# Kernel tuning notes

Measured on AMD Instinct MI355X. Metric: run time of the kernel, lower is better.

## Reference

```python
import jax, jax.numpy as jnp
import numpy as np

B, N, D, E = 8, 512, 256, 16384  # batch, num_nodes, hidden_dim, num_edges


def setup_inputs() -> dict:
    key = jax.random.key(0)
    kf, ke, k1, k2, k3, k4 = jax.random.split(key, 6)
    features = jax.random.normal(kf, (B, N, D), dtype=jnp.float32)
    edge_index = jax.random.randint(ke, (2, E), 0, N, dtype=jnp.int64)
    # weight_net: Linear(2D -> D), ReLU, Linear(D -> 1), Sigmoid
    s1 = 1.0 / np.sqrt(2 * D)
    s2 = 1.0 / np.sqrt(D)
    W1 = jax.random.uniform(k1, (2 * D, D), jnp.float32, -s1, s1)
    b1 = jax.random.uniform(k2, (D,), jnp.float32, -s1, s1)
    W2 = jax.random.uniform(k3, (D, 1), jnp.float32, -s2, s2)
    b2 = jax.random.uniform(k4, (1,), jnp.float32, -s2, s2)
    return {"features": features, "W1": W1, "b1": b1, "W2": W2, "b2": b2,
            "edge_index": edge_index}


def reference(features, W1, b1, W2, b2, edge_index):
    src, dst = edge_index[0], edge_index[1]            # [E], [E]
    fi = features[:, src]                              # [B, E, D]
    fj = features[:, dst]                              # [B, E, D]
    pair = jnp.concatenate([fi, fj], axis=-1)          # [B, E, 2D]
    h = jax.nn.relu(jnp.einsum('bef,fh->beh', pair, W1) + b1)   # [B, E, D]
    s = jax.nn.sigmoid(jnp.einsum('beh,ho->beo', h, W2) + b2)[..., 0]  # [B, E]
    bsz, n = features.shape[0], features.shape[1]
    weights = jnp.zeros((bsz, n, n), features.dtype).at[:, src, dst].set(s)
    return weights
```

## Files before the change

### kernel.cpp

```cpp
#include <hip/hip_runtime.h>
#include <hip/hip_bf16.h>
#include <cstdint>

#define B_ 8
#define N_ 512
#define D_ 256
#define E_ 16384
#define H_ 256

#define SA_STRIDE 56
#define SB_STRIDE 56
#define BCAP 128

using bf16x8 = __attribute__((ext_vector_type(8))) short;
using f32x4  = __attribute__((ext_vector_type(4))) float;

__device__ inline unsigned short f2bf(float f) {
    union { float f; unsigned u; } v; v.f = f;
    unsigned u = v.u;
    return (unsigned short)((u + 0x7fffu + ((u >> 16) & 1u)) >> 16);
}

__global__ __launch_bounds__(256)
void prep_k(const float* __restrict__ W1, unsigned short* __restrict__ W1T,
            int* __restrict__ gCount) {
    __shared__ float tile[64][65];
    const int tb = blockIdx.x, t = threadIdx.x;
    if (tb == 32) {
        gCount[t] = 0;
        gCount[t + 256] = 0;
        return;
    }
    const int h   = tb >> 4;
    const int rem = tb & 15;
    const int tk  = (rem >> 2) * 64;
    const int tn  = (rem & 3) * 64;
    const float* Wh = W1 + (size_t)h * 256 * 256;
    const int c = t & 63, r0 = t >> 6;
#pragma unroll
    for (int i = 0; i < 16; i++) {
        int r = r0 + i * 4;
        tile[r][c] = Wh[(size_t)(tk + r) * 256 + tn + c];
    }
    __syncthreads();
#pragma unroll
    for (int i = 0; i < 16; i++) {
        int rn = r0 + i * 4;
        W1T[(size_t)(h * 256 + tn + rn) * 256 + tk + c] = f2bf(tile[c][rn]);
    }
}

__global__ __launch_bounds__(256)
void node_gemm(const float* __restrict__ feat,
               const unsigned short* __restrict__ W1T,
               const float* __restrict__ b1,
               const int* __restrict__ eidx,
               unsigned short* __restrict__ P,
               float4* __restrict__ out4,
               int* __restrict__ gCount, int* __restrict__ gBucket) {
    const int t = threadIdx.x;

    if (blockIdx.x >= 128) {
        __shared__ int hist[512];
        __shared__ int base[512];
        const int sb = blockIdx.x - 128;
        int mysrc[8], mydst[8], myslot[8];
        for (int i = t; i < 512; i += 256) hist[i] = 0;
        __syncthreads();
#pragma unroll
        for (int i = 0; i < 8; i++) {
            int e = sb * 2048 + i * 256 + t;
            mysrc[i] = eidx[e];
            mydst[i] = eidx[E_ + e];
            myslot[i] = atomicAdd(&hist[mysrc[i]], 1);
        }
        __syncthreads();
        for (int i = t; i < 512; i += 256) {
            int c = hist[i];
            base[i] = c ? atomicAdd(&gCount[i], c) : 0;
        }
        __syncthreads();
#pragma unroll
        for (int i = 0; i < 8; i++)
            gBucket[(mysrc[i] << 7) + base[mysrc[i]] + myslot[i]] = mydst[i];
        return;
    }

    __shared__ unsigned short sA[64 * SA_STRIDE];
    __shared__ unsigned short sB[256 * SB_STRIDE];

    const int bm = blockIdx.x >> 1;
    const int bn = blockIdx.x & 1;
    const int m0 = bm * 64;

    {
        float4 z = make_float4(0.f, 0.f, 0.f, 0.f);
        float4* oz = out4 + (size_t)blockIdx.x * 4096 + t;
#pragma unroll
        for (int i = 0; i < 16; i++) oz[i * 256] = z;
    }

    const int arow = t >> 2;
    const int akg  = (t & 3) * 8;
    const float* pA = feat + (size_t)(m0 + arow) * 256;
    const unsigned short* pB = W1T + (size_t)(bn * 256 + t) * 256;

    const int wave = t >> 6, lane = t & 63, l15 = lane & 15, quad = lane >> 4;

    f32x4 acc[4][4];
#pragma unroll
    for (int rm = 0; rm < 4; rm++)
#pragma unroll
        for (int cn = 0; cn < 4; cn++)
            acc[rm][cn] = (f32x4){0.f, 0.f, 0.f, 0.f};

    for (int k0 = 0; k0 < 256; k0 += 32) {
        __syncthreads();
        {
            float4 lo = *(const float4*)(pA + k0 + akg);
            float4 hi = *(const float4*)(pA + k0 + akg + 4);
            union { bf16x8 v; unsigned short s[8]; } u;
            u.s[0] = f2bf(lo.x); u.s[1] = f2bf(lo.y); u.s[2] = f2bf(lo.z); u.s[3] = f2bf(lo.w);
            u.s[4] = f2bf(hi.x); u.s[5] = f2bf(hi.y); u.s[6] = f2bf(hi.z); u.s[7] = f2bf(hi.w);
            *(bf16x8*)(sA + arow * SA_STRIDE + akg) = u.v;
        }
        {
            const unsigned short* p = pB + k0;
            uint4 q0 = *(const uint4*)(p);
            uint4 q1 = *(const uint4*)(p + 8);
            uint4 q2 = *(const uint4*)(p + 16);
            uint4 q3 = *(const uint4*)(p + 24);
            *(uint4*)(sB + t * SB_STRIDE +  0) = q0;
            *(uint4*)(sB + t * SB_STRIDE +  8) = q1;
            *(uint4*)(sB + t * SB_STRIDE + 16) = q2;
            *(uint4*)(sB + t * SB_STRIDE + 24) = q3;
        }
        __syncthreads();

        bf16x8 af[4], bfr[4];
#pragma unroll
        for (int rm = 0; rm < 4; rm++)
            af[rm] = *(const bf16x8*)(sA + (rm * 16 + l15) * SA_STRIDE + quad * 8);
#pragma unroll
        for (int cn = 0; cn < 4; cn++)
            bfr[cn] = *(const bf16x8*)(sB + (wave * 64 + cn * 16 + l15) * SB_STRIDE + quad * 8);
#pragma unroll
        for (int rm = 0; rm < 4; rm++)
#pragma unroll
            for (int cn = 0; cn < 4; cn++)
                acc[rm][cn] = __builtin_amdgcn_mfma_f32_16x16x32_bf16(af[rm], bfr[cn], acc[rm][cn], 0, 0, 0);
    }

#pragma unroll
    for (int cn = 0; cn < 4; cn++) {
        int colh = wave * 64 + cn * 16 + l15;
        float bias = (bn == 0) ? b1[colh] : 0.f;
        int col = bn * 256 + colh;
#pragma unroll
        for (int rm = 0; rm < 4; rm++)
#pragma unroll
            for (int r = 0; r < 4; r++) {
                int row = m0 + rm * 16 + quad * 4 + r;
                P[(size_t)row * 512 + col] = f2bf(acc[rm][cn][r] + bias);
            }
    }
}

__device__ inline float dot8nb(uint4 qu, uint4 qv, const float* w2p) {
    unsigned us[4] = {qu.x, qu.y, qu.z, qu.w};
    unsigned vs[4] = {qv.x, qv.y, qv.z, qv.w};
    float p = 0.f;
#pragma unroll
    for (int j = 0; j < 4; j++) {
        float ulo = __uint_as_float(us[j] << 16);
        float uhi = __uint_as_float(us[j] & 0xffff0000u);
        float vlo = __uint_as_float(vs[j] << 16);
        float vhi = __uint_as_float(vs[j] & 0xffff0000u);
        float hlo = fmaxf(ulo + vlo, 0.f);
        float hhi = fmaxf(uhi + vhi, 0.f);
        p = fmaf(hlo, w2p[2 * j],     p);
        p = fmaf(hhi, w2p[2 * j + 1], p);
    }
    return p;
}

__global__ __launch_bounds__(256)
void edge_score(const unsigned short* __restrict__ P,
                const float* __restrict__ W2, const float* __restrict__ b2,
                const int* __restrict__ gCount, const int* __restrict__ gBucket,
                float* __restrict__ out) {
    const int b     = blockIdx.x & 7;
    const int chunk = blockIdx.x >> 3;
    const int lane  = threadIdx.x & 63;
    const int wave  = threadIdx.x >> 6;
    const int g     = lane >> 4;
    const int w     = lane & 15;
    const int wid   = wave * 4 + g;
    const int s     = 2 * chunk + (wid >> 3);
    const int o     = wid & 7;

    const int en = gCount[s];
    const int* bucket = gBucket + (s << 7);

    float w2r[16];
#pragma unroll
    for (int j = 0; j < 4; j++)
        *(float4*)(w2r + 4 * j) = *(const float4*)(W2 + w * 16 + 4 * j);
    const float b2v = b2[0];

    const unsigned short* Pu = P + ((size_t)b * 512 + s) * 512 + w * 16;
    uint4 u0 = *(const uint4*)(Pu);
    uint4 u1 = *(const uint4*)(Pu + 8);
    const unsigned short* Pv = P + (size_t)b * 512 * 512 + 256 + w * 16;
    float* outb = out + ((size_t)b * 512 + s) * 512;

    int j = o;
    int dst0 = 0; uint4 v00 = {}, v01 = {};
    if (j < en) {
        dst0 = bucket[j];
        const unsigned short* pv = Pv + (size_t)dst0 * 512;
        v00 = *(const uint4*)pv; v01 = *(const uint4*)(pv + 8);
    }
    while (j < en) {
        int jn = j + 8;
        int dst1 = 0; uint4 v10 = {}, v11 = {};
        if (jn < en) {
            dst1 = bucket[jn];
            const unsigned short* pv = Pv + (size_t)dst1 * 512;
            v10 = *(const uint4*)pv; v11 = *(const uint4*)(pv + 8);
        }
        float p = dot8nb(u0, v00, w2r) + dot8nb(u1, v01, w2r + 8);
        p += __shfl_xor(p, 1);
        p += __shfl_xor(p, 2);
        p += __shfl_xor(p, 4);
        p += __shfl_xor(p, 8);
        if (w == 0) {
            float sv = 1.0f / (1.0f + __expf(-(p + b2v)));
            outb[dst0] = sv;
        }
        dst0 = dst1; v00 = v10; v01 = v11; j = jn;
    }
}

extern "C" void kernel_launch(void* const* d_in, const int* in_sizes, int n_in,
                              void* d_out, int out_size, void* d_ws, size_t ws_size,
                              hipStream_t stream) {
    const float* feat = (const float*)d_in[0];
    const float* W1   = (const float*)d_in[1];
    const float* b1   = (const float*)d_in[2];
    const float* W2   = (const float*)d_in[3];
    const float* b2   = (const float*)d_in[4];
    const int*   eidx = (const int*)d_in[5];
    float* out = (float*)d_out;

    unsigned short* W1T = (unsigned short*)d_ws;
    unsigned short* P   = (unsigned short*)((char*)d_ws + (1 << 20));
    int* gCount  = (int*)((char*)d_ws + (6 << 20));
    int* gBucket = (int*)((char*)d_ws + (6 << 20) + 4096);

    prep_k<<<33, 256, 0, stream>>>(W1, W1T, gCount);
    node_gemm<<<136, 256, 0, stream>>>(feat, W1T, b1, eidx, P, (float4*)out, gCount, gBucket);
    edge_score<<<2048, 256, 0, stream>>>(P, W2, b2, gCount, gBucket, out);
}
```

Baseline: 92.76 us.

## Fuse prep, node GEMM and edge scoring into one persistent kernel with grid barrier

New measurement: 153.6 us. 65.5% more time.

```diff
diff --git a/kernel.cpp b/kernel.cpp
--- a/kernel.cpp
+++ b/kernel.cpp
@@ -1,16 +1,12 @@
 #include <hip/hip_runtime.h>
-#include <hip/hip_bf16.h>
 #include <cstdint>
 
 #define B_ 8
 #define N_ 512
 #define D_ 256
 #define E_ 16384
-#define H_ 256
-
-#define SA_STRIDE 56
-#define SB_STRIDE 56
-#define BCAP 128
+
+#define SBK 264
 
 using bf16x8 = __attribute__((ext_vector_type(8))) short;
 using f32x4  = __attribute__((ext_vector_type(4))) float;
@@ -19,151 +15,6 @@
     union { float f; unsigned u; } v; v.f = f;
     unsigned u = v.u;
     return (unsigned short)((u + 0x7fffu + ((u >> 16) & 1u)) >> 16);
-}
-
-__global__ __launch_bounds__(256)
-void prep_k(const float* __restrict__ W1, unsigned short* __restrict__ W1T,
-            int* __restrict__ gCount) {
-    __shared__ float tile[64][65];
-    const int tb = blockIdx.x, t = threadIdx.x;
-    if (tb == 32) {
-        gCount[t] = 0;
-        gCount[t + 256] = 0;
-        return;
-    }
-    const int h   = tb >> 4;
-    const int rem = tb & 15;
-    const int tk  = (rem >> 2) * 64;
-    const int tn  = (rem & 3) * 64;
-    const float* Wh = W1 + (size_t)h * 256 * 256;
-    const int c = t & 63, r0 = t >> 6;
-#pragma unroll
-    for (int i = 0; i < 16; i++) {
-        int r = r0 + i * 4;
-        tile[r][c] = Wh[(size_t)(tk + r) * 256 + tn + c];
-    }
-    __syncthreads();
-#pragma unroll
-    for (int i = 0; i < 16; i++) {
-        int rn = r0 + i * 4;
-        W1T[(size_t)(h * 256 + tn + rn) * 256 + tk + c] = f2bf(tile[c][rn]);
-    }
-}
-
-__global__ __launch_bounds__(256)
-void node_gemm(const float* __restrict__ feat,
-               const unsigned short* __restrict__ W1T,
-               const float* __restrict__ b1,
-               const int* __restrict__ eidx,
-               unsigned short* __restrict__ P,
-               float4* __restrict__ out4,
-               int* __restrict__ gCount, int* __restrict__ gBucket) {
-    const int t = threadIdx.x;
-
-    if (blockIdx.x >= 128) {
-        __shared__ int hist[512];
-        __shared__ int base[512];
-        const int sb = blockIdx.x - 128;
-        int mysrc[8], mydst[8], myslot[8];
-        for (int i = t; i < 512; i += 256) hist[i] = 0;
-        __syncthreads();
-#pragma unroll
-        for (int i = 0; i < 8; i++) {
-            int e = sb * 2048 + i * 256 + t;
-            mysrc[i] = eidx[e];
-            mydst[i] = eidx[E_ + e];
-            myslot[i] = atomicAdd(&hist[mysrc[i]], 1);
-        }
-        __syncthreads();
-        for (int i = t; i < 512; i += 256) {
-            int c = hist[i];
-            base[i] = c ? atomicAdd(&gCount[i], c) : 0;
-        }
-        __syncthreads();
-#pragma unroll
-        for (int i = 0; i < 8; i++)
-            gBucket[(mysrc[i] << 7) + base[mysrc[i]] + myslot[i]] = mydst[i];
-        return;
-    }
-
-    __shared__ unsigned short sA[64 * SA_STRIDE];
-    __shared__ unsigned short sB[256 * SB_STRIDE];
-
-    const int bm = blockIdx.x >> 1;
-    const int bn = blockIdx.x & 1;
-    const int m0 = bm * 64;
-
-    {
-        float4 z = make_float4(0.f, 0.f, 0.f, 0.f);
-        float4* oz = out4 + (size_t)blockIdx.x * 4096 + t;
-#pragma unroll
-        for (int i = 0; i < 16; i++) oz[i * 256] = z;
-    }
-
-    const int arow = t >> 2;
-    const int akg  = (t & 3) * 8;
-    const float* pA = feat + (size_t)(m0 + arow) * 256;
-    const unsigned short* pB = W1T + (size_t)(bn * 256 + t) * 256;
-
-    const int wave = t >> 6, lane = t & 63, l15 = lane & 15, quad = lane >> 4;
-
-    f32x4 acc[4][4];
-#pragma unroll
-    for (int rm = 0; rm < 4; rm++)
-#pragma unroll
-        for (int cn = 0; cn < 4; cn++)
-            acc[rm][cn] = (f32x4){0.f, 0.f, 0.f, 0.f};
-
-    for (int k0 = 0; k0 < 256; k0 += 32) {
-        __syncthreads();
-        {
-            float4 lo = *(const float4*)(pA + k0 + akg);
-            float4 hi = *(const float4*)(pA + k0 + akg + 4);
-            union { bf16x8 v; unsigned short s[8]; } u;
-            u.s[0] = f2bf(lo.x); u.s[1] = f2bf(lo.y); u.s[2] = f2bf(lo.z); u.s[3] = f2bf(lo.w);
-            u.s[4] = f2bf(hi.x); u.s[5] = f2bf(hi.y); u.s[6] = f2bf(hi.z); u.s[7] = f2bf(hi.w);
-            *(bf16x8*)(sA + arow * SA_STRIDE + akg) = u.v;
-        }
-        {
-            const unsigned short* p = pB + k0;
-            uint4 q0 = *(const uint4*)(p);
-            uint4 q1 = *(const uint4*)(p + 8);
-            uint4 q2 = *(const uint4*)(p + 16);
-            uint4 q3 = *(const uint4*)(p + 24);
-            *(uint4*)(sB + t * SB_STRIDE +  0) = q0;
-            *(uint4*)(sB + t * SB_STRIDE +  8) = q1;
-            *(uint4*)(sB + t * SB_STRIDE + 16) = q2;
-            *(uint4*)(sB + t * SB_STRIDE + 24) = q3;
-        }
-        __syncthreads();
-
-        bf16x8 af[4], bfr[4];
-#pragma unroll
-        for (int rm = 0; rm < 4; rm++)
-            af[rm] = *(const bf16x8*)(sA + (rm * 16 + l15) * SA_STRIDE + quad * 8);
-#pragma unroll
-        for (int cn = 0; cn < 4; cn++)
-            bfr[cn] = *(const bf16x8*)(sB + (wave * 64 + cn * 16 + l15) * SB_STRIDE + quad * 8);
-#pragma unroll
-        for (int rm = 0; rm < 4; rm++)
-#pragma unroll
-            for (int cn = 0; cn < 4; cn++)
-                acc[rm][cn] = __builtin_amdgcn_mfma_f32_16x16x32_bf16(af[rm], bfr[cn], acc[rm][cn], 0, 0, 0);
-    }
-
-#pragma unroll
-    for (int cn = 0; cn < 4; cn++) {
-        int colh = wave * 64 + cn * 16 + l15;
-        float bias = (bn == 0) ? b1[colh] : 0.f;
-        int col = bn * 256 + colh;
-#pragma unroll
-        for (int rm = 0; rm < 4; rm++)
-#pragma unroll
-            for (int r = 0; r < 4; r++) {
-                int row = m0 + rm * 16 + quad * 4 + r;
-                P[(size_t)row * 512 + col] = f2bf(acc[rm][cn][r] + bias);
-            }
-    }
 }
 
 __device__ inline float dot8nb(uint4 qu, uint4 qv, const float* w2p) {
@@ -184,61 +35,184 @@
     return p;
 }
 
-__global__ __launch_bounds__(256)
-void edge_score(const unsigned short* __restrict__ P,
-                const float* __restrict__ W2, const float* __restrict__ b2,
-                const int* __restrict__ gCount, const int* __restrict__ gBucket,
-                float* __restrict__ out) {
-    const int b     = blockIdx.x & 7;
-    const int chunk = blockIdx.x >> 3;
-    const int lane  = threadIdx.x & 63;
-    const int wave  = threadIdx.x >> 6;
-    const int g     = lane >> 4;
-    const int w     = lane & 15;
-    const int wid   = wave * 4 + g;
-    const int s     = 2 * chunk + (wid >> 3);
-    const int o     = wid & 7;
-
-    const int en = gCount[s];
-    const int* bucket = gBucket + (s << 7);
-
+__device__ inline void grid_barrier(int* cnt, int* flag) {
+    __syncthreads();
+    if (threadIdx.x == 0) {
+        __threadfence();
+        int prev = __hip_atomic_fetch_add(cnt, 1, __ATOMIC_ACQ_REL,
+                                          __HIP_MEMORY_SCOPE_AGENT);
+        if (prev == (int)gridDim.x - 1) {
+            __hip_atomic_store(flag, 1, __ATOMIC_RELEASE, __HIP_MEMORY_SCOPE_AGENT);
+        } else {
+            for (int it = 0; it < (1 << 16); ++it) {
+                if (__hip_atomic_load(flag, __ATOMIC_ACQUIRE,
+                                      __HIP_MEMORY_SCOPE_AGENT) != 0) break;
+                __builtin_amdgcn_s_sleep(8);
+            }
+        }
+        __threadfence();
+    }
+    __syncthreads();
+}
+
+__global__ __launch_bounds__(256, 3)
+void fused(const float* __restrict__ feat, const float* __restrict__ W1,
+           const float* __restrict__ b1,   const float* __restrict__ W2,
+           const float* __restrict__ b2,   const int* __restrict__ eidx,
+           unsigned short* __restrict__ P,
+           int* __restrict__ gCount, int* __restrict__ gBucket,
+           int* __restrict__ gBar,   float* __restrict__ out)
+{
+    __shared__ __align__(16) char smem[33792];
+    const int bid = blockIdx.x, t = threadIdx.x;
+    const int b   = bid & 7;
+    const int loc = bid >> 3;
+    const int m0  = b * 512 + (loc >> 3) * 64;
+    const int bn  = loc & 7;
+    const int n0  = bn * 64;
+
+    if (bid < 8) {
+        int* hist = (int*)smem;
+        int* base = hist + 512;
+        int mysrc[8], mydst[8], myslot[8];
+        for (int i = t; i < 512; i += 256) hist[i] = 0;
+        __syncthreads();
+#pragma unroll
+        for (int i = 0; i < 8; i++) {
+            int e = bid * 2048 + i * 256 + t;
+            mysrc[i] = eidx[e];
+            mydst[i] = eidx[E_ + e];
+            myslot[i] = atomicAdd(&hist[mysrc[i]], 1);
+        }
+        __syncthreads();
+        for (int i = t; i < 512; i += 256) {
+            int c = hist[i];
+            base[i] = c ? atomicAdd(&gCount[i], c) : 0;
+        }
+        __syncthreads();
+#pragma unroll
+        for (int i = 0; i < 8; i++)
+            gBucket[(mysrc[i] << 7) + base[mysrc[i]] + myslot[i]] = mydst[i];
+        __syncthreads();
+    }
+
+    unsigned short* sB = (unsigned short*)smem;
+    {
+        const int h = bn >> 2, c0 = (bn & 3) * 64;
+        const int nn = t & 63, kg = t >> 6;
+        const float* Wp = W1 + ((size_t)(h * 256 + kg * 64)) * 256 + c0 + nn;
+        unsigned short* dstp = sB + nn * SBK + kg * 64;
+#pragma unroll
+        for (int o = 0; o < 8; o++) {
+            union { bf16x8 v; unsigned short s[8]; } u;
+#pragma unroll
+            for (int j = 0; j < 8; j++)
+                u.s[j] = f2bf(Wp[(size_t)(o * 8 + j) * 256]);
+            *(bf16x8*)(dstp + o * 8) = u.v;
+        }
+    }
+    __syncthreads();
+
+    const int wave = t >> 6, lane = t & 63, l15 = lane & 15, quad = lane >> 4;
+    {
+        const float* pAw = feat + (size_t)(m0 + wave * 16 + l15) * 256 + quad * 8;
+        f32x4 acc[4];
+#pragma unroll
+        for (int cn = 0; cn < 4; cn++) acc[cn] = (f32x4){0.f, 0.f, 0.f, 0.f};
+#pragma unroll
+        for (int ks = 0; ks < 8; ks++) {
+            float4 lo = *(const float4*)(pAw + ks * 32);
+            float4 hi = *(const float4*)(pAw + ks * 32 + 4);
+            union { bf16x8 v; unsigned short s[8]; } u;
+            u.s[0] = f2bf(lo.x); u.s[1] = f2bf(lo.y); u.s[2] = f2bf(lo.z); u.s[3] = f2bf(lo.w);
+            u.s[4] = f2bf(hi.x); u.s[5] = f2bf(hi.y); u.s[6] = f2bf(hi.z); u.s[7] = f2bf(hi.w);
+            bf16x8 af = u.v;
+#pragma unroll
+            for (int cn = 0; cn < 4; cn++) {
+                bf16x8 bfr = *(const bf16x8*)(sB + (cn * 16 + l15) * SBK + ks * 32 + quad * 8);
+                acc[cn] = __builtin_amdgcn_mfma_f32_16x16x32_bf16(af, bfr, acc[cn], 0, 0, 0);
+            }
+        }
+#pragma unroll
+        for (int cn = 0; cn < 4; cn++) {
+            int col = n0 + cn * 16 + l15;
+            float bias = (col < 256) ? b1[col] : 0.f;
+#pragma unroll
+            for (int r = 0; r < 4; r++) {
+                int row = m0 + wave * 16 + quad * 4 + r;
+                P[(size_t)row * 512 + col] = f2bf(acc[cn][r] + bias);
+            }
+        }
+    }
+
+    grid_barrier(gBar, gBar + 32);
+
+    float* rows = (float*)smem;
+    {
+        float4 z = make_float4(0.f, 0.f, 0.f, 0.f);
+        float4* rz = (float4*)rows;
+#pragma unroll
+        for (int i = 0; i < 4; i++) rz[t + i * 256] = z;
+    }
+    __syncthreads();
+
+    const int g = lane >> 4, w = lane & 15;
+    const int wid = wave * 4 + g;
     float w2r[16];
 #pragma unroll
     for (int j = 0; j < 4; j++)
         *(float4*)(w2r + 4 * j) = *(const float4*)(W2 + w * 16 + 4 * j);
     const float b2v = b2[0];
 
-    const unsigned short* Pu = P + ((size_t)b * 512 + s) * 512 + w * 16;
-    uint4 u0 = *(const uint4*)(Pu);
-    uint4 u1 = *(const uint4*)(Pu + 8);
-    const unsigned short* Pv = P + (size_t)b * 512 * 512 + 256 + w * 16;
-    float* outb = out + ((size_t)b * 512 + s) * 512;
-
-    int j = o;
-    int dst0 = 0; uint4 v00 = {}, v01 = {};
-    if (j < en) {
-        dst0 = bucket[j];
-        const unsigned short* pv = Pv + (size_t)dst0 * 512;
-        v00 = *(const uint4*)pv; v01 = *(const uint4*)(pv + 8);
-    }
-    while (j < en) {
-        int jn = j + 8;
-        int dst1 = 0; uint4 v10 = {}, v11 = {};
-        if (jn < en) {
-            dst1 = bucket[jn];
-            const unsigned short* pv = Pv + (size_t)dst1 * 512;
-            v10 = *(const uint4*)pv; v11 = *(const uint4*)(pv + 8);
-        }
-        float p = dot8nb(u0, v00, w2r) + dot8nb(u1, v01, w2r + 8);
-        p += __shfl_xor(p, 1);
-        p += __shfl_xor(p, 2);
-        p += __shfl_xor(p, 4);
-        p += __shfl_xor(p, 8);
-        if (w == 0) {
-            float sv = 1.0f / (1.0f + __expf(-(p + b2v)));
-            outb[dst0] = sv;
-        }
-        dst0 = dst1; v00 = v10; v01 = v11; j = jn;
+    const unsigned short* Pb = P + (size_t)b * 512 * 512;
+    const unsigned short* Pv = Pb + 256 + w * 16;
+
+#pragma unroll 1
+    for (int jb = 0; jb < 4; jb++) {
+        const int rl = jb * 2 + (wid >> 3);
+        const int s  = loc * 8 + rl;
+        const int o  = wid & 7;
+
+        const int en = gCount[s];
+        const int* bucket = gBucket + (s << 7);
+
+        const unsigned short* Pu = Pb + (size_t)s * 512 + w * 16;
+        uint4 u0 = *(const uint4*)(Pu);
+        uint4 u1 = *(const uint4*)(Pu + 8);
+        float* rowp = rows + rl * 512;
+
+        int j = o;
+        int dst0 = 0; uint4 v00 = {}, v01 = {};
+        if (j < en) {
+            dst0 = bucket[j];
+            const unsigned short* pv = Pv + (size_t)dst0 * 512;
+            v00 = *(const uint4*)pv; v01 = *(const uint4*)(pv + 8);
+        }
+        while (j < en) {
+            int jn = j + 8;
+            int dst1 = 0; uint4 v10 = {}, v11 = {};
+            if (jn < en) {
+                dst1 = bucket[jn];
+                const unsigned short* pv = Pv + (size_t)dst1 * 512;
+                v10 = *(const uint4*)pv; v11 = *(const uint4*)(pv + 8);
+            }
+            float p = dot8nb(u0, v00, w2r) + dot8nb(u1, v01, w2r + 8);
+            p += __shfl_xor(p, 1);
+            p += __shfl_xor(p, 2);
+            p += __shfl_xor(p, 4);
+            p += __shfl_xor(p, 8);
+            if (w == 0)
+                rowp[dst0] = 1.0f / (1.0f + __expf(-(p + b2v)));
+            dst0 = dst1; v00 = v10; v01 = v11; j = jn;
+        }
+    }
+    __syncthreads();
+
+    {
+        float4* dstf = (float4*)(out + ((size_t)b * 512 + (size_t)loc * 8) * 512);
+        const float4* srcf = (const float4*)rows;
+#pragma unroll
+        for (int i = 0; i < 4; i++) dstf[t + i * 256] = srcf[t + i * 256];
     }
 }
 
@@ -253,12 +227,12 @@
     const int*   eidx = (const int*)d_in[5];
     float* out = (float*)d_out;
 
-    unsigned short* W1T = (unsigned short*)d_ws;
-    unsigned short* P   = (unsigned short*)((char*)d_ws + (1 << 20));
-    int* gCount  = (int*)((char*)d_ws + (6 << 20));
-    int* gBucket = (int*)((char*)d_ws + (6 << 20) + 4096);
-
-    prep_k<<<33, 256, 0, stream>>>(W1, W1T, gCount);
-    node_gemm<<<136, 256, 0, stream>>>(feat, W1T, b1, eidx, P, (float4*)out, gCount, gBucket);
-    edge_score<<<2048, 256, 0, stream>>>(P, W2, b2, gCount, gBucket, out);
-}
+    int* gCount  = (int*)d_ws;
+    int* gBar    = (int*)((char*)d_ws + 2048);
+    int* gBucket = (int*)((char*)d_ws + 4096);
+    unsigned short* P = (unsigned short*)((char*)d_ws + (1 << 20));
+
+    hipMemsetAsync(d_ws, 0, 2560, stream);
+    fused<<<dim3(512), dim3(256), 0, stream>>>(feat, W1, b1, W2, b2, eidx,
+                                               P, gCount, gBucket, gBar, out);
+}
```
